# Kernel optimization log

Measured on AMD Instinct MI355X. Metric: run time of the kernel, lower is better.

## Reference

```python
import jax, jax.numpy as jnp
import numpy as np

B, SX, SY, D, H = 4, 4096, 4096, 1024, 64


def setup_inputs() -> dict:
    key = jax.random.key(0)
    ks = jax.random.split(key, 7)
    x = jax.random.normal(ks[0], (B, SX, D), dtype=jnp.float32)
    y = jax.random.normal(ks[1], (B, SY, D), dtype=jnp.float32)
    valid_lens_x = jax.random.randint(ks[2], (B,), 1, SX + 1).astype(jnp.int64)
    valid_lens_y = jax.random.randint(ks[3], (B,), 1, SY + 1).astype(jnp.int64)
    s = 1.0 / np.sqrt(D)
    Wq = jax.random.uniform(ks[4], (D, H), jnp.float32, -s, s)
    Wk = jax.random.uniform(ks[5], (D, H), jnp.float32, -s, s)
    Wv = jax.random.uniform(ks[6], (D, H), jnp.float32, -s, s)
    return {"x": x, "y": y, "valid_lens_x": valid_lens_x,
            "valid_lens_y": valid_lens_y, "use_causal": 1,
            "Wq": Wq, "Wk": Wk, "Wv": Wv}


def reference(x, y, valid_lens_x, valid_lens_y, use_causal, Wq, Wk, Wv):
    # projections (Linear, no bias)
    k = x @ Wk                      # [B, Sx, H]
    q = y @ Wq                      # [B, Sy, H]
    v = x @ Wv                      # [B, Sx, H]
    scale = k.shape[-1] ** -0.5
    wei = jnp.einsum('bqh,bkh->bqk', q, k) * scale   # [B, Sy, Sx]
    Sq, Sk = q.shape[1], k.shape[1]
    if use_causal:  # static python int -> tril masked_fill branch
        tril = jnp.tril(jnp.ones((Sq, Sk), dtype=bool))
        wei = jnp.where(tril[None], wei, -jnp.inf)
    # per-sample valid-length cross mask
    kmask = jnp.arange(Sk)[None, :] < valid_lens_x[:, None]   # [B, Sk]
    qmask = jnp.arange(Sq)[None, :] < valid_lens_y[:, None]   # [B, Sq]
    mask = qmask[:, :, None] & kmask[:, None, :]              # [B, Sq, Sk]
    wei = jnp.where(mask, wei, -jnp.inf)
    # NaN-safe softmax: zero out fully-masked rows
    row_mask = jnp.all(jnp.isinf(wei), axis=2, keepdims=True)  # [B, Sq, 1]
    safe = jnp.where(row_mask, 0.0, wei)
    probs = jax.nn.softmax(safe, axis=2)
    probs = jnp.where(row_mask, 0.0, probs)
    # dropout p=0.0 -> identity (eval)
    out = probs @ v                 # [B, Sy, H]
    return out
```

## Files before the change

kernel.cpp:

```cpp
#include <hip/hip_runtime.h>
#include <hip/hip_bf16.h>
#include <stdint.h>

#define BBATCH 4
#define SXN 4096
#define SYN 4096
#define DD 1024
#define HH 64

typedef float f32x4 __attribute__((ext_vector_type(4)));
typedef short bf16x8 __attribute__((ext_vector_type(8)));

static __device__ __forceinline__ unsigned short f2bf(float f) {
  unsigned int u = __float_as_uint(f);
  u += 0x7fffu + ((u >> 16) & 1u);
  return (unsigned short)(u >> 16);
}
static __device__ __forceinline__ float bf2f(unsigned short b) {
  return __uint_as_float(((unsigned int)b) << 16);
}

static __device__ __forceinline__ bf16x8 cvt8(f32x4 lo, f32x4 hi) {
  bf16x8 v;
  v[0] = (short)f2bf(lo[0]); v[1] = (short)f2bf(lo[1]);
  v[2] = (short)f2bf(lo[2]); v[3] = (short)f2bf(lo[3]);
  v[4] = (short)f2bf(hi[0]); v[5] = (short)f2bf(hi[1]);
  v[6] = (short)f2bf(hi[2]); v[7] = (short)f2bf(hi[3]);
  return v;
}

static __device__ __forceinline__ void gload_lds16(const void* g, void* l) {
  __builtin_amdgcn_global_load_lds(
      (const __attribute__((address_space(1))) unsigned int*)g,
      (__attribute__((address_space(3))) unsigned int*)l, 16, 0, 0);
}

__global__ __launch_bounds__(256) void prep_wt(
    const float* __restrict__ Wq, const float* __restrict__ Wk,
    const float* __restrict__ Wv, unsigned short* __restrict__ Wt) {
  int gid = blockIdx.x * 256 + threadIdx.x;
  int mat = gid >> 16;
  int k = gid & 1023;
  int h = (gid >> 10) & 63;
  const float* W = (mat == 0) ? Wk : (mat == 1) ? Wv : Wq;
  Wt[gid] = f2bf(W[k * HH + h]);
}

__global__ __launch_bounds__(256, 4) void proj_kernel(
    const float* __restrict__ xin, const float* __restrict__ yin,
    const unsigned short* __restrict__ Wt,
    unsigned short* __restrict__ Qb, unsigned short* __restrict__ Kb,
    unsigned short* __restrict__ Vt) {
  __shared__ __align__(16) float xa[2][64 * 64];
  const int tid = threadIdx.x;
  const int w = tid >> 6, l = tid & 63;
  const int li = l & 15, lg = l >> 4;
  const bool qpath = blockIdx.x >= 256;
  const int row0 = (qpath ? (blockIdx.x - 256) : (int)blockIdx.x) * 64;
  const float* src = qpath ? yin : xin;
  const unsigned short* WtA = qpath ? (Wt + 2 * 65536) : Wt;
  const unsigned short* WtB = Wt + 65536;

  f32x4 acc0[4], acc1[4];
  const f32x4 z4 = {0.f, 0.f, 0.f, 0.f};
#pragma unroll
  for (int i = 0; i < 4; ++i) { acc0[i] = z4; acc1[i] = z4; }

  auto stage = [&](int bsel, int kc) {
#pragma unroll
    for (int i = 0; i < 4; ++i) {
      const int r = i * 16 + w * 4 + (l >> 4);
      const int c16 = (l & 15) ^ (r & 7);
      const float* g = src + (size_t)(row0 + r) * DD + kc * 64 + c16 * 4;
      float* lp = &xa[bsel][i * 1024 + w * 256];
      gload_lds16(g, lp);
    }
  };

  int buf = 0;
  stage(0, 0);
  __syncthreads();
  for (int kc = 0; kc < 16; ++kc) {
    if (kc < 15) stage(buf ^ 1, kc + 1);
    const int rrow = w * 16 + li;
    const int swz = (rrow & 7) * 4;
#pragma unroll
    for (int ks = 0; ks < 2; ++ks) {
      const int base = rrow * 64 + ks * 32 + lg * 8;
      const f32x4 lo = *reinterpret_cast<const f32x4*>(&xa[buf][base ^ swz]);
      const f32x4 hi = *reinterpret_cast<const f32x4*>(&xa[buf][(base + 4) ^ swz]);
      const bf16x8 a = cvt8(lo, hi);
      const int gks = kc * 2 + ks;
      bf16x8 bA[4], bB[4];
#pragma unroll
      for (int hb = 0; hb < 4; ++hb)
        bA[hb] = *reinterpret_cast<const bf16x8*>(
            &WtA[(hb * 16 + li) * 1024 + gks * 32 + lg * 8]);
      if (!qpath) {
#pragma unroll
        for (int hb = 0; hb < 4; ++hb)
          bB[hb] = *reinterpret_cast<const bf16x8*>(
              &WtB[(hb * 16 + li) * 1024 + gks * 32 + lg * 8]);
      }
#pragma unroll
      for (int hb = 0; hb < 4; ++hb)
        acc0[hb] = __builtin_amdgcn_mfma_f32_16x16x32_bf16(a, bA[hb], acc0[hb], 0, 0, 0);
      if (!qpath) {
#pragma unroll
        for (int hb = 0; hb < 4; ++hb)
          acc1[hb] = __builtin_amdgcn_mfma_f32_16x16x32_bf16(a, bB[hb], acc1[hb], 0, 0, 0);
      }
    }
    __syncthreads();
    buf ^= 1;
  }

  const int rbase = row0 + w * 16 + lg * 4;
  if (qpath) {
#pragma unroll
    for (int hb = 0; hb < 4; ++hb)
#pragma unroll
      for (int r = 0; r < 4; ++r)
        Qb[(size_t)(rbase + r) * HH + hb * 16 + li] = f2bf(acc0[hb][r] * 0.125f);
  } else {
#pragma unroll
    for (int hb = 0; hb < 4; ++hb)
#pragma unroll
      for (int r = 0; r < 4; ++r)
        Kb[(size_t)(rbase + r) * HH + hb * 16 + li] = f2bf(acc0[hb][r]);
    const int b = rbase >> 12;
    const int sx = rbase & 4095;
#pragma unroll
    for (int hb = 0; hb < 4; ++hb) {
      ushort4 o;
      o.x = f2bf(acc1[hb][0]); o.y = f2bf(acc1[hb][1]);
      o.z = f2bf(acc1[hb][2]); o.w = f2bf(acc1[hb][3]);
      *reinterpret_cast<ushort4*>(
          &Vt[((size_t)b * HH + hb * 16 + li) * SXN + sx]) = o;
    }
  }
}

union FlashSm {
  unsigned short Pl[8][16][72];
  float Ol[8][16][64];
};

__global__ __launch_bounds__(512, 4) void flash_kernel(
    const unsigned short* __restrict__ Qb, const unsigned short* __restrict__ Kb,
    const unsigned short* __restrict__ Vt, const int* __restrict__ vlx_p,
    const int* __restrict__ vly_p, const int* __restrict__ uc_p,
    float* __restrict__ out) {
  __shared__ __align__(16) FlashSm sm;
  __shared__ float Ml[8][16], Ll[8][16];

  const int tid = threadIdx.x;
  const int w = tid >> 6, l = tid & 63;
  const int li = l & 15, lg = l >> 4;

  const int kblk = blockIdx.x;
  const int b = (kblk & 7) >> 1;
  const int g = 255 - (((kblk >> 3) << 1) | (kblk & 1));
  const int q0 = g * 16;
  const int vlx = vlx_p[b], vly = vly_p[b];
  const int causal = uc_p[0];
  const float LOG2E = 1.4426950408889634f;

  float* outB = out + (size_t)b * SYN * HH;

  if (q0 >= vly) {
    *reinterpret_cast<float2*>(&outB[(size_t)q0 * HH + tid * 2]) =
        make_float2(0.f, 0.f);
    return;
  }

  int kend = causal ? min(vlx, q0 + 16) : vlx;
  if (kend > SXN) kend = SXN;
  const int nst = (kend + 63) >> 6;
  const int s0 = (w * nst) >> 3;
  const int s1 = ((w + 1) * nst) >> 3;

  const unsigned short* KbB = Kb + (size_t)b * SXN * HH;
  const unsigned short* VtB = Vt + (size_t)b * HH * SXN;

  f32x4 o[4];
  float mrun[4], lrun[4];
  const f32x4 z4 = {0.f, 0.f, 0.f, 0.f};
#pragma unroll
  for (int i = 0; i < 4; ++i) { o[i] = z4; mrun[i] = -INFINITY; lrun[i] = 0.f; }

  const int qg0 = q0 + lg * 4;

  if (s1 > s0) {
    const unsigned short* Qrow = Qb + ((size_t)b * SYN + q0 + li) * HH;
    const bf16x8 qa0 = *reinterpret_cast<const bf16x8*>(&Qrow[lg * 8]);
    const bf16x8 qa1 = *reinterpret_cast<const bf16x8*>(&Qrow[32 + lg * 8]);

    for (int s = s0; s < s1; ++s) {
      const int key0 = s << 6;
      bf16x8 f[8];
#pragma unroll
      for (int kb = 0; kb < 4; ++kb) {
        const unsigned short* Kr = &KbB[(size_t)(key0 + kb * 16 + li) * HH];
        f[kb * 2] = *reinterpret_cast<const bf16x8*>(&Kr[lg * 8]);
        f[kb * 2 + 1] = *reinterpret_cast<const bf16x8*>(&Kr[32 + lg * 8]);
      }
      f32x4 sa[4];
#pragma unroll
      for (int kb = 0; kb < 4; ++kb) {
        f32x4 acc = z4;
        acc = __builtin_amdgcn_mfma_f32_16x16x32_bf16(qa0, f[kb * 2], acc, 0, 0, 0);
        acc = __builtin_amdgcn_mfma_f32_16x16x32_bf16(qa1, f[kb * 2 + 1], acc, 0, 0, 0);
        sa[kb] = acc;
      }
#pragma unroll
      for (int kh = 0; kh < 2; ++kh)
#pragma unroll
        for (int df = 0; df < 4; ++df)
          f[kh * 4 + df] = *reinterpret_cast<const bf16x8*>(
              &VtB[(size_t)(df * 16 + li) * SXN + key0 + kh * 32 + lg * 8]);

#pragma unroll
      for (int r = 0; r < 4; ++r) {
        const int qcap = causal ? (qg0 + r) : 0x7fffffff;
        float sv[4];
#pragma unroll
        for (int kb = 0; kb < 4; ++kb) {
          const int kg = key0 + kb * 16 + li;
          const bool valid = (kg < vlx) && (kg <= qcap);
          sv[kb] = valid ? sa[kb][r] : -1e30f;
        }
        float tm = fmaxf(fmaxf(sv[0], sv[1]), fmaxf(sv[2], sv[3]));
        tm = fmaxf(tm, __shfl_xor(tm, 1));
        tm = fmaxf(tm, __shfl_xor(tm, 2));
        tm = fmaxf(tm, __shfl_xor(tm, 4));
        tm = fmaxf(tm, __shfl_xor(tm, 8));
        const float mn = fmaxf(mrun[r], tm);
        const float corr = exp2f((mrun[r] - mn) * LOG2E);
        mrun[r] = mn;
        float ps = 0.f;
#pragma unroll
        for (int kb = 0; kb < 4; ++kb) {
          const float p = exp2f((sv[kb] - mn) * LOG2E);
          const unsigned short pb = f2bf(p);
          sm.Pl[w][lg * 4 + r][kb * 16 + li] = pb;
          ps += bf2f(pb);
        }
        ps += __shfl_xor(ps, 1);
        ps += __shfl_xor(ps, 2);
        ps += __shfl_xor(ps, 4);
        ps += __shfl_xor(ps, 8);
        lrun[r] = lrun[r] * corr + ps;
#pragma unroll
        for (int df = 0; df < 4; ++df) o[df][r] *= corr;
      }

#pragma unroll
      for (int kh = 0; kh < 2; ++kh) {
        const bf16x8 pa =
            *reinterpret_cast<const bf16x8*>(&sm.Pl[w][li][kh * 32 + lg * 8]);
#pragma unroll
        for (int df = 0; df < 4; ++df)
          o[df] = __builtin_amdgcn_mfma_f32_16x16x32_bf16(pa, f[kh * 4 + df],
                                                          o[df], 0, 0, 0);
      }
    }
  }

  __syncthreads();

#pragma unroll
  for (int df = 0; df < 4; ++df)
#pragma unroll
    for (int r = 0; r < 4; ++r)
      sm.Ol[w][lg * 4 + r][df * 16 + li] = o[df][r];
  if (li == 0) {
#pragma unroll
    for (int r = 0; r < 4; ++r) {
      Ml[w][lg * 4 + r] = mrun[r];
      Ll[w][lg * 4 + r] = lrun[r];
    }
  }
  __syncthreads();

  {
#pragma unroll
    for (int i = 0; i < 2; ++i) {
      const int rr = w * 2 + i;
      const int q = q0 + rr;
      float res = 0.f;
      if (q < vly) {
        float M = -INFINITY;
#pragma unroll
        for (int cc = 0; cc < 8; ++cc) M = fmaxf(M, Ml[cc][rr]);
        if (M > -1e37f) {
          float lsum = 0.f, acc = 0.f;
#pragma unroll
          for (int cc = 0; cc < 8; ++cc) {
            const float wt = exp2f((Ml[cc][rr] - M) * LOG2E);
            lsum += wt * Ll[cc][rr];
            acc += wt * sm.Ol[cc][rr][l];
          }
          res = (lsum > 0.f) ? acc / lsum : 0.f;
        }
      }
      outB[(size_t)q * HH + l] = res;
    }
  }
}

extern "C" void kernel_launch(void* const* d_in, const int* in_sizes, int n_in,
                              void* d_out, int out_size, void* d_ws, size_t ws_size,
                              hipStream_t stream) {
  const float* x = (const float*)d_in[0];
  const float* y = (const float*)d_in[1];
  const int* vlx = (const int*)d_in[2];
  const int* vly = (const int*)d_in[3];
  const int* uc = (const int*)d_in[4];
  const float* Wq = (const float*)d_in[5];
  const float* Wk = (const float*)d_in[6];
  const float* Wv = (const float*)d_in[7];
  float* out = (float*)d_out;

  char* ws = (char*)d_ws;
  unsigned short* Qb = (unsigned short*)(ws);
  unsigned short* Kb = (unsigned short*)(ws + (2u << 20));
  unsigned short* Vt = (unsigned short*)(ws + (4u << 20));
  unsigned short* Wt = (unsigned short*)(ws + (6u << 20));

  prep_wt<<<768, 256, 0, stream>>>(Wq, Wk, Wv, Wt);
  proj_kernel<<<512, 256, 0, stream>>>(x, y, Wt, Qb, Kb, Vt);
  flash_kernel<<<1024, 512, 0, stream>>>(Qb, Kb, Vt, vlx, vly, uc, out);
}
```

Before: 250.2 us.

## Load projection activations directly into registers, dropping LDS staging

The projection kernel stops staging x/y tiles through double-buffered shared memory with async global-to-LDS loads and barriers. Each wave now owns 16 rows and loads its fp32 A fragments straight from global memory into registers, ping-ponging between two register sets to prefetch the next K chunk. This removes the LDS traffic and the __syncthreads calls, and the launch bound is relaxed to 2 blocks per SM to leave room for the extra registers. The cost is that global loads are less coalesced (16-byte-per-lane strided row accesses), and occupancy may drop.

```diff
diff --git a/kernel.cpp b/kernel.cpp
--- a/kernel.cpp
+++ b/kernel.cpp
@@ -27,12 +27,6 @@
   v[4] = (short)f2bf(hi[0]); v[5] = (short)f2bf(hi[1]);
   v[6] = (short)f2bf(hi[2]); v[7] = (short)f2bf(hi[3]);
   return v;
-}
-
-static __device__ __forceinline__ void gload_lds16(const void* g, void* l) {
-  __builtin_amdgcn_global_load_lds(
-      (const __attribute__((address_space(1))) unsigned int*)g,
-      (__attribute__((address_space(3))) unsigned int*)l, 16, 0, 0);
 }
 
 __global__ __launch_bounds__(256) void prep_wt(
@@ -46,50 +40,49 @@
   Wt[gid] = f2bf(W[k * HH + h]);
 }
 
-__global__ __launch_bounds__(256, 4) void proj_kernel(
+__global__ __launch_bounds__(256, 2) void proj_kernel(
     const float* __restrict__ xin, const float* __restrict__ yin,
     const unsigned short* __restrict__ Wt,
     unsigned short* __restrict__ Qb, unsigned short* __restrict__ Kb,
     unsigned short* __restrict__ Vt) {
-  __shared__ __align__(16) float xa[2][64 * 64];
   const int tid = threadIdx.x;
   const int w = tid >> 6, l = tid & 63;
   const int li = l & 15, lg = l >> 4;
-  const bool qpath = blockIdx.x >= 256;
-  const int row0 = (qpath ? (blockIdx.x - 256) : (int)blockIdx.x) * 64;
+  const int gwave = blockIdx.x * 4 + w;
+  const bool qpath = gwave >= 1024;
+  const int row0 = (gwave & 1023) * 16;
   const float* src = qpath ? yin : xin;
   const unsigned short* WtA = qpath ? (Wt + 2 * 65536) : Wt;
   const unsigned short* WtB = Wt + 65536;
 
+  const float* arow = src + (size_t)(row0 + li) * DD + lg * 8;
+
   f32x4 acc0[4], acc1[4];
   const f32x4 z4 = {0.f, 0.f, 0.f, 0.f};
 #pragma unroll
   for (int i = 0; i < 4; ++i) { acc0[i] = z4; acc1[i] = z4; }
 
-  auto stage = [&](int bsel, int kc) {
-#pragma unroll
-    for (int i = 0; i < 4; ++i) {
-      const int r = i * 16 + w * 4 + (l >> 4);
-      const int c16 = (l & 15) ^ (r & 7);
-      const float* g = src + (size_t)(row0 + r) * DD + kc * 64 + c16 * 4;
-      float* lp = &xa[bsel][i * 1024 + w * 256];
-      gload_lds16(g, lp);
-    }
-  };
-
-  int buf = 0;
-  stage(0, 0);
-  __syncthreads();
-  for (int kc = 0; kc < 16; ++kc) {
-    if (kc < 15) stage(buf ^ 1, kc + 1);
-    const int rrow = w * 16 + li;
-    const int swz = (rrow & 7) * 4;
+  f32x4 aldA[4], aldB[4];
+
+#pragma unroll
+  for (int ks = 0; ks < 2; ++ks) {
+    aldA[ks * 2]     = *reinterpret_cast<const f32x4*>(arow + ks * 32);
+    aldA[ks * 2 + 1] = *reinterpret_cast<const f32x4*>(arow + ks * 32 + 4);
+  }
+
+#pragma unroll 1
+  for (int kc2 = 0; kc2 < 8; ++kc2) {
+    const int kc = kc2 * 2;
+    {
+      const float* nrow = arow + (size_t)(kc + 1) * 64;
+#pragma unroll
+      for (int ks = 0; ks < 2; ++ks) {
+        aldB[ks * 2]     = *reinterpret_cast<const f32x4*>(nrow + ks * 32);
+        aldB[ks * 2 + 1] = *reinterpret_cast<const f32x4*>(nrow + ks * 32 + 4);
+      }
+    }
 #pragma unroll
     for (int ks = 0; ks < 2; ++ks) {
-      const int base = rrow * 64 + ks * 32 + lg * 8;
-      const f32x4 lo = *reinterpret_cast<const f32x4*>(&xa[buf][base ^ swz]);
-      const f32x4 hi = *reinterpret_cast<const f32x4*>(&xa[buf][(base + 4) ^ swz]);
-      const bf16x8 a = cvt8(lo, hi);
       const int gks = kc * 2 + ks;
       bf16x8 bA[4], bB[4];
 #pragma unroll
@@ -102,6 +95,7 @@
           bB[hb] = *reinterpret_cast<const bf16x8*>(
               &WtB[(hb * 16 + li) * 1024 + gks * 32 + lg * 8]);
       }
+      const bf16x8 a = cvt8(aldA[ks * 2], aldA[ks * 2 + 1]);
 #pragma unroll
       for (int hb = 0; hb < 4; ++hb)
         acc0[hb] = __builtin_amdgcn_mfma_f32_16x16x32_bf16(a, bA[hb], acc0[hb], 0, 0, 0);
@@ -111,11 +105,41 @@
           acc1[hb] = __builtin_amdgcn_mfma_f32_16x16x32_bf16(a, bB[hb], acc1[hb], 0, 0, 0);
       }
     }
-    __syncthreads();
-    buf ^= 1;
-  }
-
-  const int rbase = row0 + w * 16 + lg * 4;
+    if (kc2 < 7) {
+      const float* nrow = arow + (size_t)(kc + 2) * 64;
+#pragma unroll
+      for (int ks = 0; ks < 2; ++ks) {
+        aldA[ks * 2]     = *reinterpret_cast<const f32x4*>(nrow + ks * 32);
+        aldA[ks * 2 + 1] = *reinterpret_cast<const f32x4*>(nrow + ks * 32 + 4);
+      }
+    }
+#pragma unroll
+    for (int ks = 0; ks < 2; ++ks) {
+      const int gks = (kc + 1) * 2 + ks;
+      bf16x8 bA[4], bB[4];
+#pragma unroll
+      for (int hb = 0; hb < 4; ++hb)
+        bA[hb] = *reinterpret_cast<const bf16x8*>(
+            &WtA[(hb * 16 + li) * 1024 + gks * 32 + lg * 8]);
+      if (!qpath) {
+#pragma unroll
+        for (int hb = 0; hb < 4; ++hb)
+          bB[hb] = *reinterpret_cast<const bf16x8*>(
+              &WtB[(hb * 16 + li) * 1024 + gks * 32 + lg * 8]);
+      }
+      const bf16x8 a = cvt8(aldB[ks * 2], aldB[ks * 2 + 1]);
+#pragma unroll
+      for (int hb = 0; hb < 4; ++hb)
+        acc0[hb] = __builtin_amdgcn_mfma_f32_16x16x32_bf16(a, bA[hb], acc0[hb], 0, 0, 0);
+      if (!qpath) {
+#pragma unroll
+        for (int hb = 0; hb < 4; ++hb)
+          acc1[hb] = __builtin_amdgcn_mfma_f32_16x16x32_bf16(a, bB[hb], acc1[hb], 0, 0, 0);
+      }
+    }
+  }
+
+  const int rbase = row0 + lg * 4;
   if (qpath) {
 #pragma unroll
     for (int hb = 0; hb < 4; ++hb)
```

Result: no change. 248.2 us (-0.8%).
